# Kernel tuning notes

Hardware: AMD Instinct MI355X
Metric: run time of the kernel (lower is better)

The kernel has to match this reference:

```python
import jax, jax.numpy as jnp
import numpy as np

WEIGHT = 1.0
SIM_THRESHOLD = 0.8


def setup_inputs() -> dict:
    key = jax.random.key(0)
    k1, k2, k3, k4 = jax.random.split(key, 4)
    B, E, H, C = 8192, 16, 1024, 128  # batch, num_experts, hidden, clusters
    routing_probs = jax.random.normal(k1, (B, E), dtype=jnp.float32)
    # Clustered embeddings so some pairs exceed the similarity threshold:
    # intra-cluster cosine sim ~ 1024/(1024 + 0.09*1024) ~ 0.92 > 0.8.
    centers = jax.random.normal(k2, (C, H), dtype=jnp.float32)
    assign = jax.random.randint(k3, (B,), 0, C)
    input_embeddings = centers[assign] + 0.3 * jax.random.normal(k4, (B, H), dtype=jnp.float32)
    return {"routing_probs": routing_probs, "input_embeddings": input_embeddings}


def reference(routing_probs, input_embeddings):
    B = routing_probs.shape[0]
    # L2-normalize embeddings and build pairwise cosine similarity [B, B]
    emb = input_embeddings / jnp.linalg.norm(input_embeddings, axis=-1, keepdims=True)
    sim = emb @ emb.T
    mask = (sim > SIM_THRESHOLD) & ~jnp.eye(B, dtype=bool)
    # Batch-wide softmax/log_softmax computed once (fuses the per-pair loop)
    L = jax.nn.log_softmax(routing_probs, axis=-1)  # [B, E]
    P = jnp.exp(L)                                   # [B, E]
    neg_entropy = jnp.sum(P * L, axis=-1)            # [B], sum_k p_j log p_j
    # kl[i, j] = KL(P_j || P_i) = sum_k P_j (log P_j - L_i)
    kl = neg_entropy[None, :] - L @ P.T              # [B, B]
    cnt = jnp.sum(mask)
    loss = jnp.where(
        cnt > 0,
        jnp.sum(jnp.where(mask, kl, 0.0)) / jnp.maximum(cnt, 1).astype(kl.dtype),
        jnp.array(0.0, dtype=kl.dtype),
    )
    return WEIGHT * loss
```

## Files before the change

### kernel.cpp

```cpp
#include <hip/hip_runtime.h>
#include <hip/hip_bf16.h>
#include <math.h>

#define B_SZ 8192
#define H_SZ 1024
#define E_SZ 16
#define SIM_THR_I 12903
typedef float floatx4 __attribute__((ext_vector_type(4)));
typedef int   intx4   __attribute__((ext_vector_type(4)));

#define OFF_NE   4096
#define OFF_L    65536
#define OFF_P    (65536 + 524288)
#define OFF_EMB  2097152


__device__ __forceinline__ void gload16(const void* g, void* l) {
    __builtin_amdgcn_global_load_lds(
        (const __attribute__((address_space(1))) void*)g,
        (__attribute__((address_space(3))) void*)l, 16, 0, 0);
}

__device__ __forceinline__ unsigned int pack4_i8(float4 v, float s) {
    int a = (int)rintf(v.x * s), b = (int)rintf(v.y * s);
    int c = (int)rintf(v.z * s), d = (int)rintf(v.w * s);
    return (a & 255) | ((b & 255) << 8) | ((c & 255) << 16) | ((d & 255) << 24);
}

__global__ __launch_bounds__(256)
void prep_kernel(const float* __restrict__ rp,
                 const float* __restrict__ emb,
                 unsigned char* __restrict__ out8,
                 float* __restrict__ L, float* __restrict__ P,
                 float* __restrict__ ne,
                 float* __restrict__ gsum, unsigned int* __restrict__ gcnt,
                 unsigned int* __restrict__ done) {
    const int b = blockIdx.x;
    const int tid = threadIdx.x;
    if (b < 512) {
        __shared__ __align__(16) unsigned char stage[16 * 1040];
        const int wave = tid >> 6, lane = tid & 63;
        const int g = b;
#pragma unroll
        for (int t = 0; t < 4; t++) {
            int r = g * 16 + wave * 4 + t;
            const float4* row4 = (const float4*)(emb + (size_t)r * H_SZ);
            float4 v0 = row4[lane * 4 + 0], v1 = row4[lane * 4 + 1];
            float4 v2 = row4[lane * 4 + 2], v3 = row4[lane * 4 + 3];
            float ss = v0.x*v0.x + v0.y*v0.y + v0.z*v0.z + v0.w*v0.w
                     + v1.x*v1.x + v1.y*v1.y + v1.z*v1.z + v1.w*v1.w
                     + v2.x*v2.x + v2.y*v2.y + v2.z*v2.z + v2.w*v2.w
                     + v3.x*v3.x + v3.y*v3.y + v3.z*v3.z + v3.w*v3.w;
#pragma unroll
            for (int off = 32; off > 0; off >>= 1) ss += __shfl_down(ss, off, 64);
            ss = __shfl(ss, 0, 64);
            float s = rsqrtf(ss) * 127.0f;
            uint4 c;
            c.x = pack4_i8(v0, s);
            c.y = pack4_i8(v1, s);
            c.z = pack4_i8(v2, s);
            c.w = pack4_i8(v3, s);
            *(uint4*)(stage + (r & 15) * 1040 + lane * 16) = c;
        }
        __syncthreads();
#pragma unroll
        for (int p = 0; p < 4; p++) {
            int d = p * 256 + tid;
            int m = d & 15;
            int c = (d >> 6) * 4 + ((d >> 4) & 3);
            uint4 v = *(const uint4*)(stage + m * 1040 + c * 16);
            *(uint4*)(out8 + (size_t)g * 16384 + (size_t)d * 16) = v;
        }
    } else {
        int i = (b - 512) * 256 + tid;
        if (i == 0) { *gsum = 0.f; *gcnt = 0u; *done = 0u; }
        if (i >= B_SZ) return;
        const float* x = rp + i * E_SZ;
        float v[E_SZ];
        float m = -INFINITY;
#pragma unroll
        for (int k = 0; k < E_SZ; k++) { v[k] = x[k]; m = fmaxf(m, v[k]); }
        float s = 0.f;
#pragma unroll
        for (int k = 0; k < E_SZ; k++) s += expf(v[k] - m);
        float lse = m + logf(s);
        float nent = 0.f;
#pragma unroll
        for (int k = 0; k < E_SZ; k++) {
            float l = v[k] - lse;
            float p = expf(l);
            L[i * E_SZ + k] = l;
            P[i * E_SZ + k] = p;
            nent += p * l;
        }
        ne[i] = nent;
    }
}

__global__ __launch_bounds__(1024, 2)
void sim_kl_kernel(const unsigned char* __restrict__ embL,
                   const float* __restrict__ Lm, const float* __restrict__ Pm,
                   const float* __restrict__ ne,
                   float* __restrict__ gsum, unsigned int* __restrict__ gcnt,
                   unsigned int* __restrict__ done, float* __restrict__ out) {
    __shared__ __align__(16) char smem[4][16384];
    __shared__ float redf[16];
    __shared__ unsigned int redc[16];

    const int x = blockIdx.x & 7;
    int s = blockIdx.x >> 3;
    const int phase = s & 15;
    int bjs[4] = { x, x + 8, 23 - x, 31 - x };
    int bi = 0, bj = 0;
#pragma unroll
    for (int t = 0; t < 4; t++) {
        int n = bjs[t] + 1;
        if (s < n) { bj = bjs[t]; bi = s; break; }
        s -= n;
    }
    const int rowI = bi * 256, rowJ = bj * 256;

    const int tid  = threadIdx.x;
    const int lane = tid & 63;
    const int wave = tid >> 6;
    const int wrg = wave >> 2;
    const int wcg = wave & 3;
    const int quad = lane >> 4;
    const int l16  = lane & 15;

    intx4 acc[4][4];
#pragma unroll
    for (int mi = 0; mi < 4; mi++)
#pragma unroll
        for (int ni = 0; ni < 4; ni++) {
            intx4 z = {0, 0, 0, 0};
            acc[mi][ni] = z;
        }

    const char* srcA = (const char*)embL + (size_t)(bi * 16 + wave) * 16384 + lane * 16;
    const char* srcB = (const char*)embL + (size_t)(bj * 16 + wave) * 16384 + lane * 16;
    const int gW = wave * 1024;

    {
        const int ko = phase * 1024;
        gload16(srcA + ko, smem[0] + gW);
        gload16(srcB + ko, smem[2] + gW);
    }

    const int aoff = wrg * 4096 + lane * 16;
    const int boff = wcg * 4096 + lane * 16;

    for (int kt = 0; kt < 16; kt++) {
        const int b = kt & 1;
        __syncthreads();
        if (kt + 1 < 16) {
            const int ko = (((kt + 1) + phase) & 15) * 1024;
            gload16(srcA + ko, smem[b ^ 1] + gW);
            gload16(srcB + ko, smem[2 + (b ^ 1)] + gW);
        }

        intx4 af[4], bf[4];
#pragma unroll
        for (int mi = 0; mi < 4; mi++)
            af[mi] = *(const intx4*)(smem[b] + aoff + mi * 1024);
#pragma unroll
        for (int ni = 0; ni < 4; ni++)
            bf[ni] = *(const intx4*)(smem[2 + b] + boff + ni * 1024);
#pragma unroll
        for (int mi = 0; mi < 4; mi++)
#pragma unroll
            for (int ni = 0; ni < 4; ni++)
                acc[mi][ni] = __builtin_amdgcn_mfma_i32_16x16x64_i8(
                    af[mi], bf[ni], acc[mi][ni], 0, 0, 0);
    }

    __syncthreads();
    unsigned short* wl = (unsigned short*)smem + wave * 2048;
    int base = 0;
#pragma unroll
    for (int mi = 0; mi < 4; mi++) {
#pragma unroll
        for (int ni = 0; ni < 4; ni++) {
#pragma unroll
            for (int r = 0; r < 4; r++) {
                int il = wrg * 64 + mi * 16 + quad * 4 + r;
                int jl = wcg * 64 + ni * 16 + l16;
                bool msk = (acc[mi][ni][r] > SIM_THR_I) && (rowJ + jl > rowI + il);
                unsigned long long bal = __ballot(msk);
                if (msk) {
                    int pos = base + __popcll(bal & ((1ull << lane) - 1ull));
                    if (pos < 2048) wl[pos] = (unsigned short)((il << 8) | jl);
                }
                base += __popcll(bal);
            }
        }
    }
    if (base > 2048) base = 2048;

    float fsum = 0.f;
    unsigned int lcnt = 0;
    for (int t = lane; t < base; t += 64) {
        int e = wl[t];
        int i = rowI + (e >> 8), j = rowJ + (e & 255);
        const float4* Li4 = (const float4*)(Lm + i * E_SZ);
        const float4* Pj4 = (const float4*)(Pm + j * E_SZ);
        const float4* Lj4 = (const float4*)(Lm + j * E_SZ);
        const float4* Pi4 = (const float4*)(Pm + i * E_SZ);
        float d = 0.f, d2 = 0.f;
#pragma unroll
        for (int q = 0; q < 4; q++) {
            float4 a = Li4[q], bb = Pj4[q];
            d += a.x * bb.x + a.y * bb.y + a.z * bb.z + a.w * bb.w;
            float4 a2 = Lj4[q], b2 = Pi4[q];
            d2 += a2.x * b2.x + a2.y * b2.y + a2.z * b2.z + a2.w * b2.w;
        }
        fsum += (ne[j] - d) + (ne[i] - d2);
        lcnt += 2;
    }

#pragma unroll
    for (int off = 32; off > 0; off >>= 1) {
        fsum += __shfl_down(fsum, off, 64);
        lcnt += __shfl_down(lcnt, off, 64);
    }
    if (lane == 0) { redf[wave] = fsum; redc[wave] = lcnt; }
    __syncthreads();
    if (tid == 0) {
        float sv = 0.f;
        unsigned int c = 0u;
#pragma unroll
        for (int w = 0; w < 16; w++) { sv += redf[w]; c += redc[w]; }
        if (c > 0u) {
            atomicAdd(gsum, sv);
            atomicAdd(gcnt, c);
        }
        __threadfence();
        unsigned int old = atomicAdd(done, 1u);
        if (old == gridDim.x - 1) {
            float S = atomicAdd(gsum, 0.0f);
            unsigned int C = atomicAdd(gcnt, 0u);
            out[0] = (C > 0u) ? (S / (float)C) : 0.f;
        }
    }
}

extern "C" void kernel_launch(void* const* d_in, const int* in_sizes, int n_in,
                              void* d_out, int out_size, void* d_ws, size_t ws_size,
                              hipStream_t stream) {
    const float* rp  = (const float*)d_in[0];
    const float* emb = (const float*)d_in[1];
    float* out = (float*)d_out;

    char* ws = (char*)d_ws;
    float*         gsum = (float*)(ws + 0);
    unsigned int*  gcnt = (unsigned int*)(ws + 4);
    unsigned int*  done = (unsigned int*)(ws + 8);
    float*         ne   = (float*)(ws + OFF_NE);
    float*         Lm   = (float*)(ws + OFF_L);
    float*         Pm   = (float*)(ws + OFF_P);
    unsigned char* embL = (unsigned char*)(ws + OFF_EMB);

    prep_kernel<<<512 + 32, 256, 0, stream>>>(rp, emb, embL, Lm, Pm, ne, gsum, gcnt, done);
    sim_kl_kernel<<<528, 1024, 0, stream>>>(embL, Lm, Pm, ne, gsum, gcnt, done, out);
}
```

Baseline: 147.8 us.

## Deepen LDS prefetch pipeline to four slots with explicit vmcnt waits

Replaces the double-buffered LDS staging of the int8 similarity GEMM with a four-slot ring that keeps three K-tiles in flight. It uses hand-written s_waitcnt vmcnt plus s_barrier instead of __syncthreads, and fully unrolls the K loop. The goal is to hide global-to-LDS load latency behind the MFMA work. In exchange, LDS per block grows to 128KB, which limits residency to one block per CU. The launch_bounds minimum-blocks hint is also raised, which may tighten the register budget and risk spills.

New measurement: 148.3 us. Within noise of the previous version (+0.3%).

```diff
diff --git a/kernel.cpp b/kernel.cpp
--- a/kernel.cpp
+++ b/kernel.cpp
@@ -97,13 +97,13 @@
     }
 }
 
-__global__ __launch_bounds__(1024, 2)
+__global__ __launch_bounds__(1024, 4)
 void sim_kl_kernel(const unsigned char* __restrict__ embL,
                    const float* __restrict__ Lm, const float* __restrict__ Pm,
                    const float* __restrict__ ne,
                    float* __restrict__ gsum, unsigned int* __restrict__ gcnt,
                    unsigned int* __restrict__ done, float* __restrict__ out) {
-    __shared__ __align__(16) char smem[4][16384];
+    __shared__ __align__(16) char smem[131072];
     __shared__ float redf[16];
     __shared__ unsigned int redc[16];
 
@@ -141,37 +141,46 @@
     const char* srcB = (const char*)embL + (size_t)(bj * 16 + wave) * 16384 + lane * 16;
     const int gW = wave * 1024;
 
-    {
-        const int ko = phase * 1024;
-        gload16(srcA + ko, smem[0] + gW);
-        gload16(srcB + ko, smem[2] + gW);
+#pragma unroll
+    for (int p = 0; p < 3; p++) {
+        const int ko = ((p + phase) & 15) * 1024;
+        gload16(srcA + ko, smem + p * 16384 + gW);
+        gload16(srcB + ko, smem + 65536 + p * 16384 + gW);
     }
 
     const int aoff = wrg * 4096 + lane * 16;
-    const int boff = wcg * 4096 + lane * 16;
-
+    const int boff = 65536 + wcg * 4096 + lane * 16;
+
+#pragma unroll
     for (int kt = 0; kt < 16; kt++) {
-        const int b = kt & 1;
-        __syncthreads();
-        if (kt + 1 < 16) {
-            const int ko = (((kt + 1) + phase) & 15) * 1024;
-            gload16(srcA + ko, smem[b ^ 1] + gW);
-            gload16(srcB + ko, smem[2 + (b ^ 1)] + gW);
-        }
-
+        if (kt < 14)
+            asm volatile("s_waitcnt vmcnt(4)\ns_barrier" ::: "memory");
+        else if (kt == 14)
+            asm volatile("s_waitcnt vmcnt(2)\ns_barrier" ::: "memory");
+        else
+            asm volatile("s_waitcnt vmcnt(0)\ns_barrier" ::: "memory");
+
+        const int slot = kt & 3;
         intx4 af[4], bf[4];
 #pragma unroll
         for (int mi = 0; mi < 4; mi++)
-            af[mi] = *(const intx4*)(smem[b] + aoff + mi * 1024);
+            af[mi] = *(const intx4*)(smem + slot * 16384 + aoff + mi * 1024);
 #pragma unroll
         for (int ni = 0; ni < 4; ni++)
-            bf[ni] = *(const intx4*)(smem[2 + b] + boff + ni * 1024);
+            bf[ni] = *(const intx4*)(smem + slot * 16384 + boff + ni * 1024);
 #pragma unroll
         for (int mi = 0; mi < 4; mi++)
 #pragma unroll
             for (int ni = 0; ni < 4; ni++)
                 acc[mi][ni] = __builtin_amdgcn_mfma_i32_16x16x64_i8(
                     af[mi], bf[ni], acc[mi][ni], 0, 0, 0);
+
+        if (kt + 3 < 16) {
+            const int ko = ((kt + 3 + phase) & 15) * 1024;
+            const int ps = (kt + 3) & 3;
+            gload16(srcA + ko, smem + ps * 16384 + gW);
+            gload16(srcB + ko, smem + 65536 + ps * 16384 + gW);
+        }
     }
 
     __syncthreads();
```

## Load GEMM fragments directly from global into registers with triple buffering

Applied to the files above, without the earlier changes.

The shared-memory staging of int8 embedding tiles, done with global_load_lds double buffering and a __syncthreads per k-step, is replaced. Each wave now loads its MFMA fragments straight from global memory into registers and keeps a 3-deep register prefetch pipeline. This removes the LDS traffic and the block-wide barriers in the main loop. In exchange, operands shared across waves are loaded redundantly from global/L2, register pressure rises, and the cross-block phase staggering of k-offsets is dropped.

Result: slower. 172.7 us (+16.8%).

```diff
diff --git a/kernel.cpp b/kernel.cpp
--- a/kernel.cpp
+++ b/kernel.cpp
@@ -14,12 +14,6 @@
 #define OFF_P    (65536 + 524288)
 #define OFF_EMB  2097152
 
-
-__device__ __forceinline__ void gload16(const void* g, void* l) {
-    __builtin_amdgcn_global_load_lds(
-        (const __attribute__((address_space(1))) void*)g,
-        (__attribute__((address_space(3))) void*)l, 16, 0, 0);
-}
 
 __device__ __forceinline__ unsigned int pack4_i8(float4 v, float s) {
     int a = (int)rintf(v.x * s), b = (int)rintf(v.y * s);
@@ -103,13 +97,12 @@
                    const float* __restrict__ ne,
                    float* __restrict__ gsum, unsigned int* __restrict__ gcnt,
                    unsigned int* __restrict__ done, float* __restrict__ out) {
-    __shared__ __align__(16) char smem[4][16384];
+    __shared__ unsigned short list[16][2048];
     __shared__ float redf[16];
     __shared__ unsigned int redc[16];
 
     const int x = blockIdx.x & 7;
     int s = blockIdx.x >> 3;
-    const int phase = s & 15;
     int bjs[4] = { x, x + 8, 23 - x, 31 - x };
     int bi = 0, bj = 0;
 #pragma unroll
@@ -137,45 +130,39 @@
             acc[mi][ni] = z;
         }
 
-    const char* srcA = (const char*)embL + (size_t)(bi * 16 + wave) * 16384 + lane * 16;
-    const char* srcB = (const char*)embL + (size_t)(bj * 16 + wave) * 16384 + lane * 16;
-    const int gW = wave * 1024;
-
-    {
-        const int ko = phase * 1024;
-        gload16(srcA + ko, smem[0] + gW);
-        gload16(srcB + ko, smem[2] + gW);
-    }
-
-    const int aoff = wrg * 4096 + lane * 16;
-    const int boff = wcg * 4096 + lane * 16;
-
+    const char* pA = (const char*)embL + (size_t)(bi * 16 + wrg * 4) * 16384 + lane * 16;
+    const char* pB = (const char*)embL + (size_t)(bj * 16 + wcg * 4) * 16384 + lane * 16;
+
+    intx4 fa[3][4], fb[3][4];
+#pragma unroll
+    for (int p = 0; p < 3; p++) {
+#pragma unroll
+        for (int mi = 0; mi < 4; mi++) {
+            fa[p][mi] = *(const intx4*)(pA + mi * 16384 + p * 1024);
+            fb[p][mi] = *(const intx4*)(pB + mi * 16384 + p * 1024);
+        }
+    }
+
+#pragma unroll
     for (int kt = 0; kt < 16; kt++) {
-        const int b = kt & 1;
-        __syncthreads();
-        if (kt + 1 < 16) {
-            const int ko = (((kt + 1) + phase) & 15) * 1024;
-            gload16(srcA + ko, smem[b ^ 1] + gW);
-            gload16(srcB + ko, smem[2 + (b ^ 1)] + gW);
-        }
-
-        intx4 af[4], bf[4];
-#pragma unroll
-        for (int mi = 0; mi < 4; mi++)
-            af[mi] = *(const intx4*)(smem[b] + aoff + mi * 1024);
-#pragma unroll
-        for (int ni = 0; ni < 4; ni++)
-            bf[ni] = *(const intx4*)(smem[2 + b] + boff + ni * 1024);
+        const int buf = kt % 3;
 #pragma unroll
         for (int mi = 0; mi < 4; mi++)
 #pragma unroll
             for (int ni = 0; ni < 4; ni++)
                 acc[mi][ni] = __builtin_amdgcn_mfma_i32_16x16x64_i8(
-                    af[mi], bf[ni], acc[mi][ni], 0, 0, 0);
-    }
-
-    __syncthreads();
-    unsigned short* wl = (unsigned short*)smem + wave * 2048;
+                    fa[buf][mi], fb[buf][ni], acc[mi][ni], 0, 0, 0);
+        if (kt + 3 < 16) {
+            const int ko = (kt + 3) * 1024;
+#pragma unroll
+            for (int mi = 0; mi < 4; mi++) {
+                fa[buf][mi] = *(const intx4*)(pA + mi * 16384 + ko);
+                fb[buf][mi] = *(const intx4*)(pB + mi * 16384 + ko);
+            }
+        }
+    }
+
+    unsigned short* wl = list[wave];
     int base = 0;
 #pragma unroll
     for (int mi = 0; mi < 4; mi++) {
```
